# Optimization experiments

Hardware: AMD Instinct MI355X
Metric: run time of the kernel (lower is better)

The kernel has to match this reference:

```python
import jax, jax.numpy as jnp
import numpy as np

B, T, C = 1, 2048, 2048
H, N = 16, 128            # num_attention_heads, head_size
KVH = 4                   # num_key_value_heads
N_REP = H // KVH
D_DECAY, D_AAA, D_MV, D_MK, D_GATE = 160, 96, 64, 64, 160
ROPE_THETA = 1000000.0
EPS = 1e-6

def _rms_norm(h, w):
    var = jnp.mean(jnp.square(h.astype(jnp.float32)), axis=-1, keepdims=True)
    return (w * (h.astype(jnp.float32) * jax.lax.rsqrt(var + EPS))).astype(h.dtype)

def _rotate_half(q):
    q1, q2 = jnp.split(q, 2, axis=-1)
    return jnp.concatenate([-q2, q1], axis=-1)

def setup_inputs():
    key = jax.random.key(0)
    ks = jax.random.split(key, 24)
    f = jnp.float32
    rn = lambda k, shape, s=1.0: jax.random.normal(k, shape, dtype=f) * s
    half = N // 2
    inv_freq = 1.0 / (ROPE_THETA ** (jnp.arange(half, dtype=f) / half))
    freqs = jnp.arange(T, dtype=f)[:, None] * inv_freq[None, :]
    emb = jnp.concatenate([freqs, freqs], axis=-1)
    return {
        "x": rn(ks[0], (B, T, C)),
        "v_first": rn(ks[1], (B, T, KVH, N)),
        "k_first": rn(ks[2], (B, T, KVH, N)),
        "attention_mask": jnp.ones((B, T), f),
        "cos": jnp.cos(emb)[None],
        "sin": jnp.sin(emb)[None],
        "w0": rn(ks[3], (1, 1, H * N), 0.5) - 2.0,
        "w1": rn(ks[4], (C, D_DECAY), 0.02),
        "w2": rn(ks[5], (D_DECAY, H * N), 0.02),
        "a0": rn(ks[6], (1, 1, H * N), 0.1),
        "a1": rn(ks[7], (C, D_AAA), 0.02),
        "a2": rn(ks[8], (D_AAA, H * N), 0.02),
        "v0": rn(ks[9], (1, 1, KVH * N), 0.1) + 0.73,
        "v1": rn(ks[10], (C, D_MV), 0.02),
        "v2": rn(ks[11], (D_MV, KVH * N), 0.02),
        "k0": rn(ks[12], (1, 1, KVH * N), 0.1) + 0.73,
        "k1": rn(ks[13], (C, D_MK), 0.02),
        "k2": rn(ks[14], (D_MK, KVH * N), 0.02),
        "g1": rn(ks[15], (C, D_GATE), 0.02),
        "g2": rn(ks[16], (D_GATE, H * N), 0.02),
        "r_k": rn(ks[17], (H, N), 0.02) - 0.04,
        "r_norm_w": jnp.ones((N,), f),
        "k_norm_w": jnp.ones((N,), f),
        "W_r": rn(ks[18], (C, H * N), 0.02),
        "W_k": rn(ks[19], (C, KVH * N), 0.02),
        "W_v": rn(ks[20], (C, KVH * N), 0.02),
        "W_o": rn(ks[21], (H * N, C), 0.02),
    }

def _forward(x, v_first, k_first, attention_mask, cos, sin, w0, w1, w2, a0, a1, a2,
             v0, v1, v2, k0, k1, k2, g1, g2, r_k, r_norm_w, k_norm_w, W_r, W_k, W_v, W_o):
    xm = x * attention_mask[..., None]
    r = _rms_norm((xm @ W_r).reshape(B, T, H, N), r_norm_w)
    k = _rms_norm((xm @ W_k).reshape(B, T, KVH, N), k_norm_w)
    v = (xm @ W_v).reshape(B, T, KVH, N)
    c, s = cos[:, :, None, :], sin[:, :, None, :]   # rope, unsqueeze_dim=2
    r = r * c + _rotate_half(r) * s
    k = k * c + _rotate_half(k) * s
    w = -jax.nn.softplus(-(w0 + jnp.tanh(xm @ w1) @ w2)) - 0.5   # (B,T,H*N), always <= -0.5
    a = jax.nn.sigmoid(a0 + (xm @ a1) @ a2).reshape(B, T, H, N)  # in-context learning rate
    g = jax.nn.sigmoid(xm @ g1) @ g2                             # output gate (B,T,H*N)
    # residual mixing with first-layer value/key (layer_id > 0 branch)
    v = v + (v_first - v) * jax.nn.sigmoid(v0 + (xm @ v1) @ v2).reshape(B, T, KVH, N)
    k = k + (k_first - k) * jax.nn.sigmoid(k0 + (xm @ k1) @ k2).reshape(B, T, KVH, N)
    k = jnp.repeat(k, N_REP, axis=2)   # GQA repeat_kv -> (B,T,H,N)
    v = jnp.repeat(v, N_REP, axis=2)
    kk = k / jnp.maximum(jnp.linalg.norm(k, axis=-1, keepdims=True), 1e-12)  # F.normalize
    aa, bb = -kk, kk * a               # rank-1 state-update vectors
    wdec = jnp.exp(-jnp.exp(w.reshape(B, T, H, N)))  # per-channel decay in (0,1)

    def step(S, xs):                   # RWKV-7 state recurrence; S: (B,H,N,N) value x key
        wt, rt, kt, vt, at, bt = xs    # each (B,H,N)
        sa = jnp.einsum('bhij,bhj->bhi', S, at)
        S = S * wt[:, :, None, :] + sa[..., None] * bt[:, :, None, :] + vt[..., None] * kt[:, :, None, :]
        return S, jnp.einsum('bhij,bhj->bhi', S, rt)

    S0 = jnp.zeros((B, H, N, N), jnp.float32)
    xs = tuple(jnp.moveaxis(t, 1, 0) for t in (wdec, r, k, v, aa, bb))  # time-major
    _, y = jax.lax.scan(step, S0, xs)
    y = jnp.moveaxis(y, 0, 1)          # (B,T,H,N)
    y = y + jnp.sum(r * k * r_k, axis=-1, keepdims=True) * v   # r_k bonus term
    return (y.reshape(B, T, H * N) * g) @ W_o

def reference(x, v_first, k_first, attention_mask, cos, sin, w0, w1, w2, a0, a1, a2,
              v0, v1, v2, k0, k1, k2, g1, g2, r_k, r_norm_w, k_norm_w, W_r, W_k, W_v, W_o):
    return _forward(x, v_first, k_first, attention_mask, cos, sin, w0, w1, w2, a0, a1, a2,
                    v0, v1, v2, k0, k1, k2, g1, g2, r_k, r_norm_w, k_norm_w, W_r, W_k, W_v, W_o)
```

## Files before the change

### kernel.cpp

```cpp
#include <hip/hip_runtime.h>
#include <hip/hip_bf16.h>
#include <math.h>

#define T_   2048
#define C_   2048
#define H_   16
#define N_   128
#define KVH_ 4

typedef __bf16 bf16x8 __attribute__((ext_vector_type(8)));
typedef __bf16 bf16x4 __attribute__((ext_vector_type(4)));
typedef float  f32x4  __attribute__((ext_vector_type(4)));

#define MFMA16(a, b, c) __builtin_amdgcn_mfma_f32_16x16x32_bf16(a, b, c, 0, 0, 0)

static __device__ __forceinline__ float wave_sum_shfl(float v) {
#pragma unroll
    for (int m = 32; m >= 1; m >>= 1) v += __shfl_xor(v, m, 64);
    return v;
}
static __device__ __forceinline__ float block_sum_128(float v, float* sh2) {
    v = wave_sum_shfl(v);
    if ((threadIdx.x & 63) == 0) sh2[threadIdx.x >> 6] = v;
    __syncthreads();
    float r = sh2[0] + sh2[1];
    __syncthreads();
    return r;
}

__global__ void xm_to_bf16(const float* __restrict__ x, const float* __restrict__ mask,
                           __bf16* __restrict__ o) {
    int idx = blockIdx.x * 256 + threadIdx.x;
    int e = idx * 4;
    float4 v = *(const float4*)(x + e);
    float m = mask[e >> 11];
    bf16x4 r;
    r.x = (__bf16)(v.x * m); r.y = (__bf16)(v.y * m);
    r.z = (__bf16)(v.z * m); r.w = (__bf16)(v.w * m);
    *(bf16x4*)(o + e) = r;
}

struct TrDesc { const float* src; __bf16* dst; int R, C, tileStart; };
struct TrBatch { TrDesc d[13]; int n; };

__global__ void transpose_batch(TrBatch tb) {
    int bid = blockIdx.x;
    int e = 0;
    while (e + 1 < tb.n && tb.d[e + 1].tileStart <= bid) e++;
    const float* src = tb.d[e].src;
    __bf16* dst = tb.d[e].dst;
    int R = tb.d[e].R, C = tb.d[e].C;
    int tix = bid - tb.d[e].tileStart;
    int tilesC = (C + 31) >> 5;
    int trow = tix / tilesC, tcol = tix - trow * tilesC;
    int r0 = trow * 32, c0 = tcol * 32;
    __shared__ float tile[32][33];
    int tx = threadIdx.x & 31, ty = threadIdx.x >> 5;
#pragma unroll
    for (int i = 0; i < 4; i++) {
        int r = r0 + ty + i * 8, c = c0 + tx;
        if (r < R && c < C) tile[ty + i * 8][tx] = src[(size_t)r * C + c];
    }
    __syncthreads();
#pragma unroll
    for (int i = 0; i < 4; i++) {
        int c = c0 + ty + i * 8, r = r0 + tx;
        if (c < C && r < R) dst[(size_t)c * R + r] = (__bf16)tile[tx][ty + i * 8];
    }
}

__global__ void transpose_f32_bf16(const float* __restrict__ src, __bf16* __restrict__ dst,
                                   int R, int C) {
    __shared__ float tile[32][33];
    int tx = threadIdx.x & 31, ty = threadIdx.x >> 5;
    int c0 = blockIdx.x * 32, r0 = blockIdx.y * 32;
#pragma unroll
    for (int i = 0; i < 4; i++) {
        int r = r0 + ty + i * 8, c = c0 + tx;
        if (r < R && c < C) tile[ty + i * 8][tx] = src[(size_t)r * C + c];
    }
    __syncthreads();
#pragma unroll
    for (int i = 0; i < 4; i++) {
        int c = c0 + ty + i * 8, r = r0 + tx;
        if (c < C && r < R) dst[(size_t)c * R + r] = (__bf16)tile[tx][ty + i * 8];
    }
}

template <int MODE>
__global__ __launch_bounds__(256, 2)
void gemm_bf16(const __bf16* __restrict__ A, int lda, const __bf16* __restrict__ BT,
               const float* __restrict__ bias, float* __restrict__ Cf,
               __bf16* __restrict__ Cb, int N, int K, int act) {
    constexpr int LDK = 40;
    __shared__ __align__(16) __bf16 As[128 * LDK];
    __shared__ __align__(16) __bf16 Bs[128 * LDK];
    const int tid = threadIdx.x;
    const int lane = tid & 63, wave = tid >> 6;
    const int bm = blockIdx.y * 128, bn = blockIdx.x * 128;
    const int wm = (wave >> 1) * 64, wn = (wave & 1) * 64;
    const int srow = tid >> 1;
    const int skoff = (tid & 1) * 16;
    const __bf16* Ap = A + (size_t)(bm + srow) * lda + skoff;
    const __bf16* Bp = BT + (size_t)(bn + srow) * K + skoff;
    const bool bok = (bn + srow) < N;
    __bf16* AsW = As + srow * LDK + skoff;
    __bf16* BsW = Bs + srow * LDK + skoff;
    const int lm = lane & 15, lq = lane >> 4;
    f32x4 acc[4][4] = {};
    for (int k0 = 0; k0 < K; k0 += 32) {
        int4 a0 = *(const int4*)(Ap);
        int4 a1 = *(const int4*)(Ap + 8);
        int4 b0 = {0, 0, 0, 0}, b1 = {0, 0, 0, 0};
        if (bok) { b0 = *(const int4*)(Bp); b1 = *(const int4*)(Bp + 8); }
        __syncthreads();
        *(int4*)(AsW) = a0; *(int4*)(AsW + 8) = a1;
        *(int4*)(BsW) = b0; *(int4*)(BsW + 8) = b1;
        __syncthreads();
        bf16x8 af[4], bfr[4];
#pragma unroll
        for (int i = 0; i < 4; i++)
            af[i] = *(const bf16x8*)(As + (wm + i * 16 + lm) * LDK + lq * 8);
#pragma unroll
        for (int j = 0; j < 4; j++)
            bfr[j] = *(const bf16x8*)(Bs + (wn + j * 16 + lm) * LDK + lq * 8);
#pragma unroll
        for (int i = 0; i < 4; i++)
#pragma unroll
            for (int j = 0; j < 4; j++)
                acc[i][j] = MFMA16(af[i], bfr[j], acc[i][j]);
        Ap += 32; Bp += 32;
    }
#pragma unroll
    for (int j = 0; j < 4; j++) {
        int col = bn + wn + j * 16 + lm;
        if (col >= N) continue;
        float bv = (MODE == 0 && bias) ? bias[col] : 0.f;
#pragma unroll
        for (int i = 0; i < 4; i++) {
            int row0 = bm + wm + i * 16 + lq * 4;
#pragma unroll
            for (int rg = 0; rg < 4; rg++) {
                float v = acc[i][j][rg] + bv;
                int row = row0 + rg;
                if (MODE == 0) {
                    if (act == 1) v = tanhf(v);
                    else if (act == 2) v = 1.f / (1.f + __expf(-v));
                    Cf[(size_t)row * N + col] = v;
                } else {
                    if (col < 3072) {
                        Cf[(size_t)row * 3072 + col] = v;
                    } else {
                        float vv = v;
                        if (col < 3232) vv = tanhf(v);
                        else if (col >= 3456) vv = 1.f / (1.f + __expf(-v));
                        Cb[(size_t)row * 544 + (col - 3072)] = (__bf16)vv;
                    }
                }
            }
        }
    }
}

__global__ __launch_bounds__(128)
void prep_kv(float* __restrict__ mega, float* __restrict__ kkO,
             const float* __restrict__ kfirst, const float* __restrict__ vfirst,
             const float* __restrict__ kmix, const float* __restrict__ vmix,
             const float* __restrict__ cosT, const float* __restrict__ sinT,
             const float* __restrict__ knw) {
    __shared__ float sh[128];
    __shared__ float sh2[2];
    int b = blockIdx.x;
    int t = b >> 2, kvh = b & 3;
    int n = threadIdx.x;
    size_t kbase = (size_t)t * 3072 + 2048 + kvh * 128;
    size_t vbase = (size_t)t * 3072 + 2560 + kvh * 128;
    size_t fbase = (size_t)t * 512 + kvh * 128;
    float x = mega[kbase + n];
    float ssq = block_sum_128(x * x, sh2);
    float kn = knw[n] * (x * rsqrtf(ssq * (1.f / 128.f) + 1e-6f));
    sh[n] = kn;
    __syncthreads();
    float rot = (n < 64) ? -sh[n + 64] : sh[n - 64];
    float c = cosT[(size_t)t * 128 + n], s = sinT[(size_t)t * 128 + n];
    float kr = kn * c + rot * s;
    float kf = kr + (kfirst[fbase + n] - kr) * kmix[fbase + n];
    float s2 = block_sum_128(kf * kf, sh2);
    float kkv = kf / fmaxf(sqrtf(s2), 1e-12f);
    float vv = mega[vbase + n];
    float vf = vv + (vfirst[fbase + n] - vv) * vmix[fbase + n];
    mega[kbase + n] = kf;
    kkO[fbase + n] = kkv;
    mega[vbase + n] = vf;
}

__global__ __launch_bounds__(128)
void prep_r(float* __restrict__ mega, float* __restrict__ Wl,
            const float* __restrict__ rk, float* __restrict__ cOut,
            const float* __restrict__ cosT, const float* __restrict__ sinT,
            const float* __restrict__ rnw) {
    __shared__ float sh[128];
    __shared__ float sh2[2];
    int b = blockIdx.x;
    int t = b >> 4, h = b & 15;
    int kv = h >> 2;
    int n = threadIdx.x;
    size_t rbase = (size_t)t * 3072 + h * 128;
    float x = mega[rbase + n];
    float ssq = block_sum_128(x * x, sh2);
    float rn = rnw[n] * (x * rsqrtf(ssq * (1.f / 128.f) + 1e-6f));
    sh[n] = rn;
    __syncthreads();
    float rot = (n < 64) ? -sh[n + 64] : sh[n - 64];
    float c = cosT[(size_t)t * 128 + n], s = sinT[(size_t)t * 128 + n];
    float rr = rn * c + rot * s;
    mega[rbase + n] = rr;
    size_t wb_ = (size_t)t * 2048 + h * 128 + n;
    float z = Wl[wb_];
    float nz = -z;
    float sp = fmaxf(nz, 0.f) + log1pf(expf(-fabsf(nz)));
    float w = -sp - 0.5f;
    Wl[wb_] = expf(-expf(w));
    float pc = rr * mega[(size_t)t * 3072 + 2048 + kv * 128 + n] * rk[h * 128 + n];
    float cs = block_sum_128(pc, sh2);
    if (n == 0) cOut[b] = cs;
}


__global__ __launch_bounds__(64)
void scan_phaseA(const float* __restrict__ Wl, const float* __restrict__ megaF,
                 const float* __restrict__ aS, const float* __restrict__ kkB,
                 __bf16* __restrict__ ATt_g, __bf16* __restrict__ Rr_g,
                 __bf16* __restrict__ Bnt_g, __bf16* __restrict__ Knt_g,
                 __bf16* __restrict__ Vt_g, __bf16* __restrict__ Gbt_g,
                 __bf16* __restrict__ Gkt_g, float* __restrict__ Cloc_g,
                 float* __restrict__ cwL_g) {
    __shared__ __align__(16) __bf16 pool[27648];
    __bf16* Arm = pool;
    __bf16* Brm = pool + 4352;
    __bf16* Krm = pool + 8704;
    __bf16* Rrm = pool + 13056;
    __bf16* Vt  = pool + 17408;
    __bf16* Mrm = pool + 22528;
    __bf16* Mt  = pool + 23808;
    __bf16* Prm = pool + 25088;
    __bf16* Gtmp= pool + 26368;
    __bf16* M2rm = pool + 4352;
    __bf16* M2t  = pool + 5632;
    __bf16* Xa   = pool + 6912;
    __bf16* Xb   = pool + 8192;
    __bf16* Tt   = pool + 9472;
    __bf16* PTt  = pool + 10752;

    const int l = threadIdx.x, lm = l & 15, lq = l >> 4;
    const int u = blockIdx.x, h = u >> 6, c = u & 63, kv = h >> 2;
    const int n0 = l, n1 = l + 64;

    float cw0 = 1.f, cw1 = 1.f;
    for (int t = 0; t < 32; ++t) {
        int tg = c * 32 + t;
        size_t hb = (size_t)tg * 2048 + h * 128;
        size_t mb = (size_t)tg * 3072;
        size_t kb = (size_t)tg * 512 + kv * 128;
        float wv0 = Wl[hb + n0], wv1 = Wl[hb + n1];
        float r0 = megaF[mb + h * 128 + n0], r1 = megaF[mb + h * 128 + n1];
        float q0 = kkB[kb + n0], q1 = kkB[kb + n1];
        float s0 = aS[hb + n0], s1 = aS[hb + n1];
        float k0 = megaF[mb + 2048 + kv * 128 + n0], k1 = megaF[mb + 2048 + kv * 128 + n1];
        float v0 = megaF[mb + 2560 + kv * 128 + n0], v1 = megaF[mb + 2560 + kv * 128 + n1];
        float cp0 = cw0, cp1 = cw1;
        cw0 *= wv0; cw1 *= wv1;
        float ic0 = 1.f / cw0, ic1 = 1.f / cw1;
        Arm[t * 136 + n0] = (__bf16)(-cp0 * q0);
        Arm[t * 136 + n1] = (__bf16)(-cp1 * q1);
        Brm[t * 136 + n0] = (__bf16)(q0 * s0 * ic0);
        Brm[t * 136 + n1] = (__bf16)(q1 * s1 * ic1);
        Krm[t * 136 + n0] = (__bf16)(k0 * ic0);
        Krm[t * 136 + n1] = (__bf16)(k1 * ic1);
        Rrm[t * 136 + n0] = (__bf16)(cw0 * r0);
        Rrm[t * 136 + n1] = (__bf16)(cw1 * r1);
        Vt[n0 * 40 + t] = (__bf16)v0;
        Vt[n1 * 40 + t] = (__bf16)v1;
    }
    cwL_g[(size_t)u * 128 + n0] = cw0;
    cwL_g[(size_t)u * 128 + n1] = cw1;
    __syncthreads();

    auto mmLL = [&](const __bf16* Ao, const __bf16* Bo, bool incl, __bf16* dTr, __bf16* dDir) {
#pragma unroll
        for (int ri = 0; ri < 2; ri++)
#pragma unroll
        for (int ci = 0; ci < 2; ci++) {
            f32x4 acc = {};
#pragma unroll
            for (int s = 0; s < 4; s++) {
                bf16x8 af = *(const bf16x8*)(Ao + (ri * 16 + lm) * 136 + s * 32 + lq * 8);
                bf16x8 bf = *(const bf16x8*)(Bo + (ci * 16 + lm) * 136 + s * 32 + lq * 8);
                acc = MFMA16(af, bf, acc);
            }
#pragma unroll
            for (int rg = 0; rg < 4; rg++) {
                int rr = ri * 16 + lq * 4 + rg, cc = ci * 16 + lm;
                bool keep = incl ? (cc <= rr) : (cc < rr);
                __bf16 bv = (__bf16)(keep ? acc[rg] : 0.f);
                if (dTr)  dTr[cc * 40 + rr] = bv;
                if (dDir) dDir[rr * 40 + cc] = bv;
            }
        }
    };
    mmLL(Arm, Brm, false, Mrm, Mt);
    mmLL(Arm, Krm, false, Prm, nullptr);
    mmLL(Rrm, Brm, true, nullptr, Gtmp);
    __syncthreads();
    for (int i = l; i < 512; i += 64) {
        int r = i >> 4, cp = i & 15;
        ((int*)(Gbt_g + (size_t)u * 1024))[i] = *(const int*)(Gtmp + r * 40 + cp * 2);
    }
    __syncthreads();
    mmLL(Rrm, Krm, true, nullptr, Gtmp);
    __syncthreads();
    for (int i = l; i < 512; i += 64) {
        int r = i >> 4, cp = i & 15;
        ((int*)(Gkt_g + (size_t)u * 1024))[i] = *(const int*)(Gtmp + r * 40 + cp * 2);
    }
    for (int i = l; i < 2048; i += 64) {
        int t = i >> 6, cp = i & 63;
        ((int*)(Rr_g + (size_t)u * 4096))[i] = *(const int*)(Rrm + t * 136 + cp * 2);
    }
    for (int i = l; i < 2048; i += 64) {
        int n = i >> 4, tp = i & 15;
        unsigned int lo = ((const unsigned short*)Brm)[(2 * tp) * 136 + n];
        unsigned int hi = ((const unsigned short*)Brm)[(2 * tp + 1) * 136 + n];
        ((unsigned int*)(Bnt_g + (size_t)u * 4096))[i] = lo | (hi << 16);
        unsigned int lo2 = ((const unsigned short*)Krm)[(2 * tp) * 136 + n];
        unsigned int hi2 = ((const unsigned short*)Krm)[(2 * tp + 1) * 136 + n];
        ((unsigned int*)(Knt_g + (size_t)u * 4096))[i] = lo2 | (hi2 << 16);
    }
    for (int i = l; i < 2048; i += 64) {
        int n = i >> 4, tp = i & 15;
        ((int*)(Vt_g + (size_t)u * 4096))[i] = *(const int*)(Vt + n * 40 + tp * 2);
    }
    __syncthreads();

    for (int i = l; i < 1024; i += 64) {
        int s = i >> 5, t = i & 31;
        Xa[s * 40 + t] = (s == t) ? (__bf16)1.f : Mrm[s * 40 + t];
    }
    __syncthreads();

    auto mat32 = [&](const __bf16* Ao, const __bf16* Bo, const __bf16* accIn,
                     __bf16* oRm, __bf16* oT) {
#pragma unroll
        for (int ri = 0; ri < 2; ri++)
#pragma unroll
        for (int ci = 0; ci < 2; ci++) {
            f32x4 acc = {};
            if (accIn) {
#pragma unroll
                for (int rg = 0; rg < 4; rg++)
                    acc[rg] = (float)accIn[(ri * 16 + lq * 4 + rg) * 40 + ci * 16 + lm];
            }
            bf16x8 af = *(const bf16x8*)(Ao + (ri * 16 + lm) * 40 + lq * 8);
            bf16x8 bf = *(const bf16x8*)(Bo + (ci * 16 + lm) * 40 + lq * 8);
            acc = MFMA16(af, bf, acc);
#pragma unroll
            for (int rg = 0; rg < 4; rg++) {
                int rr = ri * 16 + lq * 4 + rg, cc = ci * 16 + lm;
                __bf16 bv = (__bf16)acc[rg];
                if (oRm) oRm[rr * 40 + cc] = bv;
                if (oT)  oT[cc * 40 + rr] = bv;
            }
        }
        __syncthreads();
    };
    mat32(Mrm, Mt, nullptr, M2rm, M2t);
    mat32(Xa, M2t, Xa, Xb, nullptr);
    mat32(M2rm, M2t, nullptr, Mrm, Mt);
    mat32(Xb, Mt, Xb, Xa, nullptr);
    mat32(Mrm, Mt, nullptr, M2rm, M2t);
    mat32(Xa, M2t, Xa, Xb, nullptr);
    mat32(M2rm, M2t, nullptr, Mrm, Mt);
    mat32(Xb, Mt, Xb, nullptr, Tt);
    mat32(Tt, Prm, nullptr, PTt, nullptr);

    for (int t2 = 0; t2 < 32; ++t2) {
        float a0 = 0.f, a1 = 0.f;
        for (int s = 0; s <= t2; ++s) {
            float tv = (float)Tt[t2 * 40 + s];
            a0 += tv * (float)Arm[s * 136 + n0];
            a1 += tv * (float)Arm[s * 136 + n1];
        }
        ATt_g[(size_t)u * 4096 + t2 * 128 + n0] = (__bf16)a0;
        ATt_g[(size_t)u * 4096 + t2 * 128 + n1] = (__bf16)a1;
    }
#pragma unroll
    for (int ii = 0; ii < 8; ii++)
#pragma unroll
    for (int ti = 0; ti < 2; ti++) {
        f32x4 acc = {};
        bf16x8 af = *(const bf16x8*)(Vt + (ii * 16 + lm) * 40 + lq * 8);
        bf16x8 bf = *(const bf16x8*)(PTt + (ti * 16 + lm) * 40 + lq * 8);
        acc = MFMA16(af, bf, acc);
#pragma unroll
        for (int rg = 0; rg < 4; rg++)
            Cloc_g[(size_t)u * 4096 + (ii * 16 + lq * 4 + rg) * 32 + ti * 16 + lm] = acc[rg];
    }
}

struct Ops {
    bf16x8 at[8], bn[8], kn[8], vf;
    f32x4 cl[2];
    float cw[8];
};

__global__ __launch_bounds__(64, 1)
void scan_phaseB(const __bf16* __restrict__ ATt_g, const __bf16* __restrict__ Bnt_g,
                 const __bf16* __restrict__ Knt_g, const __bf16* __restrict__ Vt_g,
                 const float* __restrict__ Cloc_g, const float* __restrict__ cwL_g,
                 __bf16* __restrict__ Sg, __bf16* __restrict__ Cg) {
    __shared__ __align__(16) __bf16 Sbf[16 * 136];
    __shared__ __align__(16) __bf16 Cbf[16 * 40];
    const int h = blockIdx.y, i0 = blockIdx.x * 16;
    const int l = threadIdx.x, lm = l & 15, lq = l >> 4;
    f32x4 st[8];
#pragma unroll
    for (int cc = 0; cc < 8; cc++) st[cc] = (f32x4){0.f, 0.f, 0.f, 0.f};

    auto loadOps = [&](int c, Ops& o) {
        size_t u = (size_t)h * 64 + c;
        const __bf16* ATp = ATt_g + u * 4096;
        const __bf16* Bp  = Bnt_g + u * 4096;
        const __bf16* Kp  = Knt_g + u * 4096;
#pragma unroll
        for (int ti = 0; ti < 2; ti++)
#pragma unroll
            for (int s = 0; s < 4; s++)
                o.at[ti * 4 + s] = *(const bf16x8*)(ATp + (ti * 16 + lm) * 128 + s * 32 + lq * 8);
#pragma unroll
        for (int cc = 0; cc < 8; cc++) {
            o.bn[cc] = *(const bf16x8*)(Bp + (cc * 16 + lm) * 32 + lq * 8);
            o.kn[cc] = *(const bf16x8*)(Kp + (cc * 16 + lm) * 32 + lq * 8);
        }
        o.vf = *(const bf16x8*)(Vt_g + u * 4096 + (i0 + lm) * 32 + lq * 8);
#pragma unroll
        for (int ti = 0; ti < 2; ti++)
#pragma unroll
            for (int rg = 0; rg < 4; rg++)
                o.cl[ti][rg] = Cloc_g[u * 4096 + (i0 + lq * 4 + rg) * 32 + ti * 16 + lm];
#pragma unroll
        for (int cc = 0; cc < 8; cc++) o.cw[cc] = cwL_g[u * 128 + cc * 16 + lm];
    };

    auto computeChunk = [&](int c, const Ops& o) {
        size_t u = (size_t)h * 64 + c;
#pragma unroll
        for (int cc = 0; cc < 8; cc++)
#pragma unroll
            for (int rg = 0; rg < 4; rg++)
                Sbf[(lq * 4 + rg) * 136 + cc * 16 + lm] = (__bf16)st[cc][rg];
        __syncthreads();
        bf16x8 saf[4];
#pragma unroll
        for (int s = 0; s < 4; s++)
            saf[s] = *(const bf16x8*)(Sbf + lm * 136 + s * 32 + lq * 8);
        f32x4 cacc[2];
#pragma unroll
        for (int ti = 0; ti < 2; ti++) {
            f32x4 acc = o.cl[ti];
#pragma unroll
            for (int s = 0; s < 4; s++) acc = MFMA16(saf[s], o.at[ti * 4 + s], acc);
            cacc[ti] = acc;
        }
#pragma unroll
        for (int ti = 0; ti < 2; ti++)
#pragma unroll
            for (int rg = 0; rg < 4; rg++)
                Cbf[(lq * 4 + rg) * 40 + ti * 16 + lm] = (__bf16)cacc[ti][rg];
        __syncthreads();
        bf16x8 cf = *(const bf16x8*)(Cbf + lm * 40 + lq * 8);
#pragma unroll
        for (int s = 0; s < 4; s++)
            *(bf16x8*)(Sg + u * 16384 + (size_t)(i0 + lm) * 128 + s * 32 + lq * 8) = saf[s];
        *(bf16x8*)(Cg + u * 4096 + (size_t)(i0 + lm) * 32 + lq * 8) = cf;
#pragma unroll
        for (int cc = 0; cc < 8; cc++) {
            st[cc] = MFMA16(cf, o.bn[cc], st[cc]);
            st[cc] = MFMA16(o.vf, o.kn[cc], st[cc]);
#pragma unroll
            for (int rg = 0; rg < 4; rg++) st[cc][rg] *= o.cw[cc];
        }
        __syncthreads();
    };

    Ops A, B;
    loadOps(0, A);
    loadOps(1, B);
    for (int c = 0; c < 64; c += 2) {
        computeChunk(c, A);
        if (c + 2 < 64) loadOps(c + 2, A);
        computeChunk(c + 1, B);
        if (c + 3 < 64) loadOps(c + 3, B);
    }
}

__global__ __launch_bounds__(64)
void scan_phaseC(const __bf16* __restrict__ Sg, const __bf16* __restrict__ Cg,
                 const __bf16* __restrict__ Rr_g, const __bf16* __restrict__ Vt_g,
                 const __bf16* __restrict__ Gbt_g, const __bf16* __restrict__ Gkt_g,
                 const float* __restrict__ cB, const float* __restrict__ megaF,
                 const float* __restrict__ gB, __bf16* __restrict__ out) {
    __shared__ float Ybuf[32 * 18];
    const int bx = blockIdx.x, h = blockIdx.y;
    const int c = bx >> 3, i0 = (bx & 7) * 16;
    const int l = threadIdx.x, lm = l & 15, lq = l >> 4;
    const size_t u = (size_t)h * 64 + c;
    bf16x8 saf[4];
#pragma unroll
    for (int s = 0; s < 4; s++)
        saf[s] = *(const bf16x8*)(Sg + u * 16384 + (size_t)(i0 + lm) * 128 + s * 32 + lq * 8);
    bf16x8 cf = *(const bf16x8*)(Cg + u * 4096 + (size_t)(i0 + lm) * 32 + lq * 8);
    bf16x8 vf = *(const bf16x8*)(Vt_g + u * 4096 + (size_t)(i0 + lm) * 32 + lq * 8);
#pragma unroll
    for (int ti = 0; ti < 2; ti++) {
        f32x4 acc = {};
#pragma unroll
        for (int s = 0; s < 4; s++) {
            bf16x8 rp = *(const bf16x8*)(Rr_g + u * 4096 + (ti * 16 + lm) * 128 + s * 32 + lq * 8);
            acc = MFMA16(saf[s], rp, acc);
        }
        bf16x8 gb = *(const bf16x8*)(Gbt_g + u * 1024 + (ti * 16 + lm) * 32 + lq * 8);
        acc = MFMA16(cf, gb, acc);
        bf16x8 gk = *(const bf16x8*)(Gkt_g + u * 1024 + (ti * 16 + lm) * 32 + lq * 8);
        acc = MFMA16(vf, gk, acc);
#pragma unroll
        for (int rg = 0; rg < 4; rg++)
            Ybuf[(ti * 16 + lm) * 18 + lq * 4 + rg] = acc[rg];
    }
    __syncthreads();
    const int kv = h >> 2;
#pragma unroll
    for (int pass = 0; pass < 8; pass++) {
        int t = pass * 4 + lq;
        int tg = c * 32 + t;
        int col = h * 128 + i0 + lm;
        float yv = Ybuf[t * 18 + lm];
        float cv = cB[tg * 16 + h];
        float vv = megaF[(size_t)tg * 3072 + 2560 + kv * 128 + i0 + lm];
        float gg = gB[(size_t)tg * 2048 + col];
        out[(size_t)tg * 2048 + col] = (__bf16)((yv + cv * vv) * gg);
    }
}

extern "C" void kernel_launch(void* const* d_in, const int* in_sizes, int n_in,
                              void* d_out, int out_size, void* d_ws, size_t ws_size,
                              hipStream_t stream) {
    (void)in_sizes; (void)n_in; (void)out_size; (void)ws_size;
    const float* x      = (const float*)d_in[0];
    const float* vfirst = (const float*)d_in[1];
    const float* kfirst = (const float*)d_in[2];
    const float* amask  = (const float*)d_in[3];
    const float* cosT   = (const float*)d_in[4];
    const float* sinT   = (const float*)d_in[5];
    const float* w0     = (const float*)d_in[6];
    const float* w1     = (const float*)d_in[7];
    const float* w2     = (const float*)d_in[8];
    const float* a0     = (const float*)d_in[9];
    const float* a1     = (const float*)d_in[10];
    const float* a2     = (const float*)d_in[11];
    const float* v0     = (const float*)d_in[12];
    const float* v1     = (const float*)d_in[13];
    const float* v2     = (const float*)d_in[14];
    const float* k0     = (const float*)d_in[15];
    const float* k1     = (const float*)d_in[16];
    const float* k2     = (const float*)d_in[17];
    const float* g1     = (const float*)d_in[18];
    const float* g2     = (const float*)d_in[19];
    const float* rk     = (const float*)d_in[20];
    const float* rnw    = (const float*)d_in[21];
    const float* knw    = (const float*)d_in[22];
    const float* W_r    = (const float*)d_in[23];
    const float* W_k    = (const float*)d_in[24];
    const float* W_v    = (const float*)d_in[25];
    const float* W_o    = (const float*)d_in[26];

    char* p = (char*)d_ws;
    auto take = [&](size_t bytes) { char* r = p; p += (bytes + 255) & ~(size_t)255; return r; };
    __bf16* arena   = (__bf16*)take((size_t)3616 * 2048 * 2);
    __bf16* xmb     = (__bf16*)take((size_t)T_ * C_ * 2);
    float*  megaF   = (float*)take((size_t)T_ * 3072 * 4);
    __bf16* megaB   = (__bf16*)take((size_t)T_ * 544 * 2);
    __bf16* w2T     = (__bf16*)take((size_t)2048 * 160 * 2);
    __bf16* a2T     = (__bf16*)take((size_t)2048 * 96 * 2);
    __bf16* v2T     = (__bf16*)take((size_t)512 * 64 * 2);
    __bf16* k2T     = (__bf16*)take((size_t)512 * 64 * 2);
    __bf16* g2T     = (__bf16*)take((size_t)2048 * 160 * 2);
    float*  Wl      = (float*)take((size_t)T_ * 2048 * 4);
    float*  aS      = (float*)take((size_t)T_ * 2048 * 4);
    float*  gB      = (float*)take((size_t)T_ * 2048 * 4);
    float*  kkB     = (float*)take((size_t)T_ * 512 * 4);
    float*  vmx     = (float*)take((size_t)T_ * 512 * 4);
    float*  kmx     = (float*)take((size_t)T_ * 512 * 4);
    float*  cB      = (float*)take((size_t)T_ * H_ * 4);
    __bf16* ATt_g   = (__bf16*)take((size_t)1024 * 4096 * 2);
    __bf16* Rr_g    = (__bf16*)take((size_t)1024 * 4096 * 2);
    __bf16* Bnt_g   = (__bf16*)take((size_t)1024 * 4096 * 2);
    __bf16* Knt_g   = (__bf16*)take((size_t)1024 * 4096 * 2);
    __bf16* Vt_g    = (__bf16*)take((size_t)1024 * 4096 * 2);
    __bf16* Gbt_g   = (__bf16*)take((size_t)1024 * 1024 * 2);
    __bf16* Gkt_g   = (__bf16*)take((size_t)1024 * 1024 * 2);
    float*  Cloc_g  = (float*)take((size_t)1024 * 4096 * 4);
    float*  cwL_g   = (float*)take((size_t)1024 * 128 * 4);
    __bf16* Sg = (__bf16*)Wl;
    __bf16* Cg = (__bf16*)kkB;

    xm_to_bf16<<<(T_ * C_ / 4) / 256, 256, 0, stream>>>(x, amask, xmb);

    TrBatch tb;
    {
        const float* srcs[13] = {W_r, W_k, W_v, w1, a1, v1, k1, g1, w2, a2, v2, k2, g2};
        __bf16* dsts[13] = {arena, arena + (size_t)2048 * 2048, arena + (size_t)2560 * 2048,
                            arena + (size_t)3072 * 2048, arena + (size_t)3232 * 2048,
                            arena + (size_t)3328 * 2048, arena + (size_t)3392 * 2048,
                            arena + (size_t)3456 * 2048, w2T, a2T, v2T, k2T, g2T};
        int Rs[13] = {2048, 2048, 2048, 2048, 2048, 2048, 2048, 2048, 160, 96, 64, 64, 160};
        int Cs[13] = {2048, 512, 512, 160, 96, 64, 64, 160, 2048, 2048, 512, 512, 2048};
        int cum = 0;
        for (int e = 0; e < 13; e++) {
            tb.d[e].src = srcs[e]; tb.d[e].dst = dsts[e];
            tb.d[e].R = Rs[e]; tb.d[e].C = Cs[e]; tb.d[e].tileStart = cum;
            cum += ((Rs[e] + 31) / 32) * ((Cs[e] + 31) / 32);
        }
        tb.n = 13;
        transpose_batch<<<cum, 256, 0, stream>>>(tb);
    }

    gemm_bf16<2><<<dim3(29, 16), 256, 0, stream>>>(xmb, 2048, arena, nullptr, megaF, megaB, 3616, 2048, 0);

    gemm_bf16<0><<<dim3(16, 16), 256, 0, stream>>>(megaB + 0,   544, w2T, w0, Wl,  nullptr, 2048, 160, 0);
    gemm_bf16<0><<<dim3(16, 16), 256, 0, stream>>>(megaB + 160, 544, a2T, a0, aS,  nullptr, 2048, 96, 2);
    gemm_bf16<0><<<dim3(4, 16),  256, 0, stream>>>(megaB + 256, 544, v2T, v0, vmx, nullptr, 512, 64, 2);
    gemm_bf16<0><<<dim3(4, 16),  256, 0, stream>>>(megaB + 320, 544, k2T, k0, kmx, nullptr, 512, 64, 2);
    gemm_bf16<0><<<dim3(16, 16), 256, 0, stream>>>(megaB + 384, 544, g2T, nullptr, gB, nullptr, 2048, 160, 0);

    prep_kv<<<T_ * KVH_, 128, 0, stream>>>(megaF, kkB, kfirst, vfirst, kmx, vmx, cosT, sinT, knw);
    prep_r<<<T_ * H_, 128, 0, stream>>>(megaF, Wl, rk, cB, cosT, sinT, rnw);

    scan_phaseA<<<1024, 64, 0, stream>>>(Wl, megaF, aS, kkB, ATt_g, Rr_g, Bnt_g, Knt_g,
                                         Vt_g, Gbt_g, Gkt_g, Cloc_g, cwL_g);
    scan_phaseB<<<dim3(8, 16), 64, 0, stream>>>(ATt_g, Bnt_g, Knt_g, Vt_g, Cloc_g, cwL_g, Sg, Cg);
    scan_phaseC<<<dim3(512, 16), 64, 0, stream>>>(Sg, Cg, Rr_g, Vt_g, Gbt_g, Gkt_g,
                                                  cB, megaF, gB, xmb);

    transpose_f32_bf16<<<dim3(64, 64), 256, 0, stream>>>(W_o, arena, 2048, 2048);
    gemm_bf16<0><<<dim3(16, 16), 256, 0, stream>>>(xmb, 2048, arena, nullptr, (float*)d_out, nullptr, 2048, 2048, 0);
}
```

Measured before the change: 583.8 us.

## Use direct-to-LDS loads in GEMM, group small GEMMs, MFMA-ize phaseA, split phaseB across waves

The GEMM now loads tiles with global_load_lds straight into unpadded LDS instead of staging them through registers. The five small LoRA up-projection GEMMs are merged into one grouped launch. Scan phase A computes its AT product with MFMA instead of a scalar triangular loop. Scan phase B spreads each head-slice state over four waves, which reduce partial products through shared memory, to raise parallelism on the serial chunk recurrence. Risks are LDS bank conflicts from dropping the padding, the extra cross-wave reduction and barrier in phase B, and the global_load_lds ordering semantics.

Result: faster. 503.5 us (-13.8%).

```diff
diff --git a/kernel.cpp b/kernel.cpp
--- a/kernel.cpp
+++ b/kernel.cpp
@@ -13,6 +13,11 @@
 typedef float  f32x4  __attribute__((ext_vector_type(4)));
 
 #define MFMA16(a, b, c) __builtin_amdgcn_mfma_f32_16x16x32_bf16(a, b, c, 0, 0, 0)
+
+static __device__ __forceinline__ void gll16(const __bf16* g, __bf16* l) {
+    __builtin_amdgcn_global_load_lds((const __attribute__((address_space(1))) void*)g,
+                                     (__attribute__((address_space(3))) void*)l, 16, 0, 0);
+}
 
 static __device__ __forceinline__ float wave_sum_shfl(float v) {
 #pragma unroll
@@ -92,44 +97,40 @@
 void gemm_bf16(const __bf16* __restrict__ A, int lda, const __bf16* __restrict__ BT,
                const float* __restrict__ bias, float* __restrict__ Cf,
                __bf16* __restrict__ Cb, int N, int K, int act) {
-    constexpr int LDK = 40;
-    __shared__ __align__(16) __bf16 As[128 * LDK];
-    __shared__ __align__(16) __bf16 Bs[128 * LDK];
+    __shared__ __align__(16) __bf16 As[128 * 32];
+    __shared__ __align__(16) __bf16 Bs[128 * 32];
     const int tid = threadIdx.x;
     const int lane = tid & 63, wave = tid >> 6;
     const int bm = blockIdx.y * 128, bn = blockIdx.x * 128;
     const int wm = (wave >> 1) * 64, wn = (wave & 1) * 64;
-    const int srow = tid >> 1;
-    const int skoff = (tid & 1) * 16;
-    const __bf16* Ap = A + (size_t)(bm + srow) * lda + skoff;
-    const __bf16* Bp = BT + (size_t)(bn + srow) * K + skoff;
-    const bool bok = (bn + srow) < N;
-    __bf16* AsW = As + srow * LDK + skoff;
-    __bf16* BsW = Bs + srow * LDK + skoff;
+    const int prow = lane >> 2, pk = (lane & 3) * 8;
+    const __bf16* ApA = A + (size_t)(bm + wave * 32 + prow) * lda + pk;
+    const __bf16* BpA = BT + (size_t)(bn + wave * 32 + prow) * K + pk;
+    const bool bokA = (bn + wave * 32 + prow) < N;
+    const bool bokB = (bn + wave * 32 + 16 + prow) < N;
+    __bf16* AsD = As + wave * 1024;
+    __bf16* BsD = Bs + wave * 1024;
     const int lm = lane & 15, lq = lane >> 4;
     f32x4 acc[4][4] = {};
     for (int k0 = 0; k0 < K; k0 += 32) {
-        int4 a0 = *(const int4*)(Ap);
-        int4 a1 = *(const int4*)(Ap + 8);
-        int4 b0 = {0, 0, 0, 0}, b1 = {0, 0, 0, 0};
-        if (bok) { b0 = *(const int4*)(Bp); b1 = *(const int4*)(Bp + 8); }
         __syncthreads();
-        *(int4*)(AsW) = a0; *(int4*)(AsW + 8) = a1;
-        *(int4*)(BsW) = b0; *(int4*)(BsW + 8) = b1;
+        gll16(ApA + k0, AsD);
+        gll16(ApA + (size_t)16 * lda + k0, AsD + 512);
+        if (bokA) gll16(BpA + k0, BsD);
+        if (bokB) gll16(BpA + (size_t)16 * K + k0, BsD + 512);
         __syncthreads();
         bf16x8 af[4], bfr[4];
 #pragma unroll
         for (int i = 0; i < 4; i++)
-            af[i] = *(const bf16x8*)(As + (wm + i * 16 + lm) * LDK + lq * 8);
+            af[i] = *(const bf16x8*)(As + (wm + i * 16 + lm) * 32 + lq * 8);
 #pragma unroll
         for (int j = 0; j < 4; j++)
-            bfr[j] = *(const bf16x8*)(Bs + (wn + j * 16 + lm) * LDK + lq * 8);
+            bfr[j] = *(const bf16x8*)(Bs + (wn + j * 16 + lm) * 32 + lq * 8);
 #pragma unroll
         for (int i = 0; i < 4; i++)
 #pragma unroll
             for (int j = 0; j < 4; j++)
                 acc[i][j] = MFMA16(af[i], bfr[j], acc[i][j]);
-        Ap += 32; Bp += 32;
     }
 #pragma unroll
     for (int j = 0; j < 4; j++) {
@@ -157,6 +158,66 @@
                         Cb[(size_t)row * 544 + (col - 3072)] = (__bf16)vv;
                     }
                 }
+            }
+        }
+    }
+}
+
+struct GSeg { const __bf16* BT; const float* bias; float* Cf; int aoff, K, N, act, bx0; };
+struct GB5 { GSeg s[5]; };
+
+__global__ __launch_bounds__(256, 2)
+void gemm_group(const __bf16* __restrict__ Abase, GB5 gb) {
+    __shared__ __align__(16) __bf16 As[128 * 32];
+    __shared__ __align__(16) __bf16 Bs[128 * 32];
+    int e = 0;
+    while (e + 1 < 5 && gb.s[e + 1].bx0 <= (int)blockIdx.x) e++;
+    const GSeg sg = gb.s[e];
+    const int K = sg.K, N = sg.N;
+    const __bf16* A = Abase + sg.aoff;
+    const int tid = threadIdx.x;
+    const int lane = tid & 63, wave = tid >> 6;
+    const int bm = blockIdx.y * 128, bn = (blockIdx.x - sg.bx0) * 128;
+    const int wm = (wave >> 1) * 64, wn = (wave & 1) * 64;
+    const int prow = lane >> 2, pk = (lane & 3) * 8;
+    const __bf16* ApA = A + (size_t)(bm + wave * 32 + prow) * 544 + pk;
+    const __bf16* BpA = sg.BT + (size_t)(bn + wave * 32 + prow) * K + pk;
+    __bf16* AsD = As + wave * 1024;
+    __bf16* BsD = Bs + wave * 1024;
+    const int lm = lane & 15, lq = lane >> 4;
+    f32x4 acc[4][4] = {};
+    for (int k0 = 0; k0 < K; k0 += 32) {
+        __syncthreads();
+        gll16(ApA + k0, AsD);
+        gll16(ApA + (size_t)16 * 544 + k0, AsD + 512);
+        gll16(BpA + k0, BsD);
+        gll16(BpA + (size_t)16 * K + k0, BsD + 512);
+        __syncthreads();
+        bf16x8 af[4], bfr[4];
+#pragma unroll
+        for (int i = 0; i < 4; i++)
+            af[i] = *(const bf16x8*)(As + (wm + i * 16 + lm) * 32 + lq * 8);
+#pragma unroll
+        for (int j = 0; j < 4; j++)
+            bfr[j] = *(const bf16x8*)(Bs + (wn + j * 16 + lm) * 32 + lq * 8);
+#pragma unroll
+        for (int i = 0; i < 4; i++)
+#pragma unroll
+            for (int j = 0; j < 4; j++)
+                acc[i][j] = MFMA16(af[i], bfr[j], acc[i][j]);
+    }
+#pragma unroll
+    for (int j = 0; j < 4; j++) {
+        int col = bn + wn + j * 16 + lm;
+        float bv = sg.bias ? sg.bias[col] : 0.f;
+#pragma unroll
+        for (int i = 0; i < 4; i++) {
+            int row0 = bm + wm + i * 16 + lq * 4;
+#pragma unroll
+            for (int rg = 0; rg < 4; rg++) {
+                float v = acc[i][j][rg] + bv;
+                if (sg.act == 2) v = 1.f / (1.f + __expf(-v));
+                sg.Cf[(size_t)(row0 + rg) * N + col] = v;
             }
         }
     }
@@ -251,6 +312,7 @@
     __bf16* Xb   = pool + 8192;
     __bf16* Tt   = pool + 9472;
     __bf16* PTt  = pool + 10752;
+    __bf16* Ant  = pool + 13056;
 
     const int l = threadIdx.x, lm = l & 15, lq = l >> 4;
     const int u = blockIdx.x, h = u >> 6, c = u & 63, kv = h >> 2;
@@ -346,6 +408,10 @@
         int s = i >> 5, t = i & 31;
         Xa[s * 40 + t] = (s == t) ? (__bf16)1.f : Mrm[s * 40 + t];
     }
+    for (int i = l; i < 4096; i += 64) {
+        int s = i & 31, n = i >> 5;
+        Ant[n * 32 + s] = Arm[s * 136 + n];
+    }
     __syncthreads();
 
     auto mat32 = [&](const __bf16* Ao, const __bf16* Bo, const __bf16* accIn,
@@ -383,15 +449,18 @@
     mat32(Xb, Mt, Xb, nullptr, Tt);
     mat32(Tt, Prm, nullptr, PTt, nullptr);
 
-    for (int t2 = 0; t2 < 32; ++t2) {
-        float a0 = 0.f, a1 = 0.f;
-        for (int s = 0; s <= t2; ++s) {
-            float tv = (float)Tt[t2 * 40 + s];
-            a0 += tv * (float)Arm[s * 136 + n0];
-            a1 += tv * (float)Arm[s * 136 + n1];
-        }
-        ATt_g[(size_t)u * 4096 + t2 * 128 + n0] = (__bf16)a0;
-        ATt_g[(size_t)u * 4096 + t2 * 128 + n1] = (__bf16)a1;
+#pragma unroll
+    for (int ti = 0; ti < 2; ti++) {
+        bf16x8 af = *(const bf16x8*)(Tt + (ti * 16 + lm) * 40 + lq * 8);
+#pragma unroll
+        for (int ni = 0; ni < 8; ni++) {
+            f32x4 accv = {};
+            bf16x8 bfv = *(const bf16x8*)(Ant + (ni * 16 + lm) * 32 + lq * 8);
+            accv = MFMA16(af, bfv, accv);
+#pragma unroll
+            for (int rg = 0; rg < 4; rg++)
+                ATt_g[(size_t)u * 4096 + (ti * 16 + lq * 4 + rg) * 128 + ni * 16 + lm] = (__bf16)accv[rg];
+        }
     }
 #pragma unroll
     for (int ii = 0; ii < 8; ii++)
@@ -407,98 +476,85 @@
     }
 }
 
-struct Ops {
-    bf16x8 at[8], bn[8], kn[8], vf;
+struct OpsV {
+    bf16x8 at[2], bn[2], kn[2], vf;
     f32x4 cl[2];
-    float cw[8];
+    float cw[2];
 };
 
-__global__ __launch_bounds__(64, 1)
+__global__ __launch_bounds__(256, 2)
 void scan_phaseB(const __bf16* __restrict__ ATt_g, const __bf16* __restrict__ Bnt_g,
                  const __bf16* __restrict__ Knt_g, const __bf16* __restrict__ Vt_g,
                  const float* __restrict__ Cloc_g, const float* __restrict__ cwL_g,
                  __bf16* __restrict__ Sg, __bf16* __restrict__ Cg) {
-    __shared__ __align__(16) __bf16 Sbf[16 * 136];
-    __shared__ __align__(16) __bf16 Cbf[16 * 40];
+    __shared__ __align__(16) __bf16 Ssl[4][16 * 40];
+    __shared__ __align__(16) float Pl[2][4][16 * 36];
     const int h = blockIdx.y, i0 = blockIdx.x * 16;
-    const int l = threadIdx.x, lm = l & 15, lq = l >> 4;
-    f32x4 st[8];
-#pragma unroll
-    for (int cc = 0; cc < 8; cc++) st[cc] = (f32x4){0.f, 0.f, 0.f, 0.f};
-
-    auto loadOps = [&](int c, Ops& o) {
+    const int tid = threadIdx.x, w = tid >> 6, l = tid & 63;
+    const int lm = l & 15, lq = l >> 4;
+    f32x4 st[2] = {};
+
+    auto loadOps = [&](int c, OpsV& o) {
         size_t u = (size_t)h * 64 + c;
-        const __bf16* ATp = ATt_g + u * 4096;
-        const __bf16* Bp  = Bnt_g + u * 4096;
-        const __bf16* Kp  = Knt_g + u * 4096;
-#pragma unroll
-        for (int ti = 0; ti < 2; ti++)
-#pragma unroll
-            for (int s = 0; s < 4; s++)
-                o.at[ti * 4 + s] = *(const bf16x8*)(ATp + (ti * 16 + lm) * 128 + s * 32 + lq * 8);
-#pragma unroll
-        for (int cc = 0; cc < 8; cc++) {
-            o.bn[cc] = *(const bf16x8*)(Bp + (cc * 16 + lm) * 32 + lq * 8);
-            o.kn[cc] = *(const bf16x8*)(Kp + (cc * 16 + lm) * 32 + lq * 8);
-        }
-        o.vf = *(const bf16x8*)(Vt_g + u * 4096 + (i0 + lm) * 32 + lq * 8);
-#pragma unroll
-        for (int ti = 0; ti < 2; ti++)
+#pragma unroll
+        for (int j = 0; j < 2; j++) {
+            o.at[j] = *(const bf16x8*)(ATt_g + u * 4096 + (size_t)(j * 16 + lm) * 128 + w * 32 + lq * 8);
+            o.bn[j] = *(const bf16x8*)(Bnt_g + u * 4096 + (size_t)(w * 32 + j * 16 + lm) * 32 + lq * 8);
+            o.kn[j] = *(const bf16x8*)(Knt_g + u * 4096 + (size_t)(w * 32 + j * 16 + lm) * 32 + lq * 8);
+            o.cw[j] = cwL_g[u * 128 + w * 32 + j * 16 + lm];
+        }
+        o.vf = *(const bf16x8*)(Vt_g + u * 4096 + (size_t)(i0 + lm) * 32 + lq * 8);
+        o.cl[0] = *(const f32x4*)(Cloc_g + u * 4096 + (size_t)(i0 + lm) * 32 + lq * 8);
+        o.cl[1] = *(const f32x4*)(Cloc_g + u * 4096 + (size_t)(i0 + lm) * 32 + lq * 8 + 4);
+    };
+
+    auto compute = [&](int c, const OpsV& o) {
+        size_t u = (size_t)h * 64 + c;
+        int buf = c & 1;
+#pragma unroll
+        for (int j = 0; j < 2; j++)
 #pragma unroll
             for (int rg = 0; rg < 4; rg++)
-                o.cl[ti][rg] = Cloc_g[u * 4096 + (i0 + lq * 4 + rg) * 32 + ti * 16 + lm];
-#pragma unroll
-        for (int cc = 0; cc < 8; cc++) o.cw[cc] = cwL_g[u * 128 + cc * 16 + lm];
+                Ssl[w][(lq * 4 + rg) * 40 + j * 16 + lm] = (__bf16)st[j][rg];
+        bf16x8 saf = *(const bf16x8*)(&Ssl[w][lm * 40 + lq * 8]);
+        f32x4 zz = {};
+        f32x4 pc0 = MFMA16(saf, o.at[0], zz);
+        f32x4 pc1 = MFMA16(saf, o.at[1], zz);
+        *(bf16x8*)(Sg + u * 16384 + (size_t)(i0 + lm) * 128 + w * 32 + lq * 8) = saf;
+#pragma unroll
+        for (int rg = 0; rg < 4; rg++) {
+            Pl[buf][w][(lq * 4 + rg) * 36 + lm] = pc0[rg];
+            Pl[buf][w][(lq * 4 + rg) * 36 + 16 + lm] = pc1[rg];
+        }
+        __syncthreads();
+        f32x4 s0 = o.cl[0], s1 = o.cl[1];
+#pragma unroll
+        for (int ww = 0; ww < 4; ww++) {
+            s0 += *(const f32x4*)(&Pl[buf][ww][lm * 36 + lq * 8]);
+            s1 += *(const f32x4*)(&Pl[buf][ww][lm * 36 + lq * 8 + 4]);
+        }
+        bf16x8 cf;
+#pragma unroll
+        for (int j = 0; j < 4; j++) { cf[j] = (__bf16)s0[j]; cf[4 + j] = (__bf16)s1[j]; }
+        if (w == 0)
+            *(bf16x8*)(Cg + u * 4096 + (size_t)(i0 + lm) * 32 + lq * 8) = cf;
+#pragma unroll
+        for (int j = 0; j < 2; j++) {
+            f32x4 t = MFMA16(o.vf, o.kn[j], st[j]);
+            t = MFMA16(cf, o.bn[j], t);
+            float cwv = o.cw[j];
+#pragma unroll
+            for (int rg = 0; rg < 4; rg++) st[j][rg] = t[rg] * cwv;
+        }
     };
 
-    auto computeChunk = [&](int c, const Ops& o) {
-        size_t u = (size_t)h * 64 + c;
-#pragma unroll
-        for (int cc = 0; cc < 8; cc++)
-#pragma unroll
-            for (int rg = 0; rg < 4; rg++)
-                Sbf[(lq * 4 + rg) * 136 + cc * 16 + lm] = (__bf16)st[cc][rg];
-        __syncthreads();
-        bf16x8 saf[4];
-#pragma unroll
-        for (int s = 0; s < 4; s++)
-            saf[s] = *(const bf16x8*)(Sbf + lm * 136 + s * 32 + lq * 8);
-        f32x4 cacc[2];
-#pragma unroll
-        for (int ti = 0; ti < 2; ti++) {
-            f32x4 acc = o.cl[ti];
-#pragma unroll
-            for (int s = 0; s < 4; s++) acc = MFMA16(saf[s], o.at[ti * 4 + s], acc);
-            cacc[ti] = acc;
-        }
-#pragma unroll
-        for (int ti = 0; ti < 2; ti++)
-#pragma unroll
-            for (int rg = 0; rg < 4; rg++)
-                Cbf[(lq * 4 + rg) * 40 + ti * 16 + lm] = (__bf16)cacc[ti][rg];
-        __syncthreads();
-        bf16x8 cf = *(const bf16x8*)(Cbf + lm * 40 + lq * 8);
-#pragma unroll
-        for (int s = 0; s < 4; s++)
-            *(bf16x8*)(Sg + u * 16384 + (size_t)(i0 + lm) * 128 + s * 32 + lq * 8) = saf[s];
-        *(bf16x8*)(Cg + u * 4096 + (size_t)(i0 + lm) * 32 + lq * 8) = cf;
-#pragma unroll
-        for (int cc = 0; cc < 8; cc++) {
-            st[cc] = MFMA16(cf, o.bn[cc], st[cc]);
-            st[cc] = MFMA16(o.vf, o.kn[cc], st[cc]);
-#pragma unroll
-            for (int rg = 0; rg < 4; rg++) st[cc][rg] *= o.cw[cc];
-        }
-        __syncthreads();
-    };
-
-    Ops A, B;
+    OpsV A, B;
     loadOps(0, A);
     loadOps(1, B);
     for (int c = 0; c < 64; c += 2) {
-        computeChunk(c, A);
+        compute(c, A);
         if (c + 2 < 64) loadOps(c + 2, A);
-        computeChunk(c + 1, B);
+        compute(c + 1, B);
         if (c + 3 < 64) loadOps(c + 3, B);
     }
 }
@@ -636,18 +692,20 @@
 
     gemm_bf16<2><<<dim3(29, 16), 256, 0, stream>>>(xmb, 2048, arena, nullptr, megaF, megaB, 3616, 2048, 0);
 
-    gemm_bf16<0><<<dim3(16, 16), 256, 0, stream>>>(megaB + 0,   544, w2T, w0, Wl,  nullptr, 2048, 160, 0);
-    gemm_bf16<0><<<dim3(16, 16), 256, 0, stream>>>(megaB + 160, 544, a2T, a0, aS,  nullptr, 2048, 96, 2);
-    gemm_bf16<0><<<dim3(4, 16),  256, 0, stream>>>(megaB + 256, 544, v2T, v0, vmx, nullptr, 512, 64, 2);
-    gemm_bf16<0><<<dim3(4, 16),  256, 0, stream>>>(megaB + 320, 544, k2T, k0, kmx, nullptr, 512, 64, 2);
-    gemm_bf16<0><<<dim3(16, 16), 256, 0, stream>>>(megaB + 384, 544, g2T, nullptr, gB, nullptr, 2048, 160, 0);
+    GB5 gb;
+    gb.s[0] = {w2T, w0, Wl,  0,   160, 2048, 0, 0};
+    gb.s[1] = {a2T, a0, aS,  160, 96,  2048, 2, 16};
+    gb.s[2] = {v2T, v0, vmx, 256, 64,  512,  2, 32};
+    gb.s[3] = {k2T, k0, kmx, 320, 64,  512,  2, 36};
+    gb.s[4] = {g2T, nullptr, gB, 384, 160, 2048, 0, 40};
+    gemm_group<<<dim3(56, 16), 256, 0, stream>>>(megaB, gb);
 
     prep_kv<<<T_ * KVH_, 128, 0, stream>>>(megaF, kkB, kfirst, vfirst, kmx, vmx, cosT, sinT, knw);
     prep_r<<<T_ * H_, 128, 0, stream>>>(megaF, Wl, rk, cB, cosT, sinT, rnw);
 
     scan_phaseA<<<1024, 64, 0, stream>>>(Wl, megaF, aS, kkB, ATt_g, Rr_g, Bnt_g, Knt_g,
                                          Vt_g, Gbt_g, Gkt_g, Cloc_g, cwL_g);
-    scan_phaseB<<<dim3(8, 16), 64, 0, stream>>>(ATt_g, Bnt_g, Knt_g, Vt_g, Cloc_g, cwL_g, Sg, Cg);
+    scan_phaseB<<<dim3(8, 16), 256, 0, stream>>>(ATt_g, Bnt_g, Knt_g, Vt_g, Cloc_g, cwL_g, Sg, Cg);
     scan_phaseC<<<dim3(512, 16), 64, 0, stream>>>(Sg, Cg, Rr_g, Vt_g, Gbt_g, Gkt_g,
                                                   cB, megaF, gB, xmb);
 
```
